# Kernel optimization log

Measured on AMD Instinct MI355X. Metric: run time of the kernel, lower is better.

## Reference

```python
import jax, jax.numpy as jnp
import numpy as np

K = 20  # neighbors


def _knn_idx(x, k):
    # x: (B, N, C). pairwise_distance[b,i,j] = -||x_i - x_j||^2; topk -> k nearest (incl. self)
    inner = jnp.einsum('bic,bjc->bij', x, x)            # (B, N, N)
    sq = jnp.sum(x * x, axis=-1)                         # (B, N)
    pd = 2.0 * inner - sq[:, :, None] - sq[:, None, :]   # (B, N, N)
    return jax.lax.top_k(pd, k)[1]                       # (B, N, k) int32


def _gather_neighbors(x, idx):
    # Faithful to source: flatten to (B*N, C) and index with per-batch indices in [0, N).
    # This means every batch gathers from batch 0's rows (bug in original, reproduced).
    B, N, C = x.shape
    flat = x.reshape(B * N, C)
    return flat[idx.reshape(-1)].reshape(B, N, idx.shape[-1], C)  # (B, N, k, C)


def setup_inputs() -> dict:
    key = jax.random.key(0)
    ks = jax.random.split(key, 11)
    B, N = 8, 4096
    emb_dim = 1024
    s = 0.05
    inp = {
        'x':  jax.random.normal(ks[0], (B, N, 3), dtype=jnp.float32),
        'w1': jax.random.normal(ks[1], (3, 64), dtype=jnp.float32) * s,
        'b1': jax.random.normal(ks[2], (64,), dtype=jnp.float32) * s,
        'w2': jax.random.normal(ks[3], (64, 64), dtype=jnp.float32) * s,
        'b2': jax.random.normal(ks[4], (64,), dtype=jnp.float32) * s,
        'w3': jax.random.normal(ks[5], (64, 64), dtype=jnp.float32) * s,
        'b3': jax.random.normal(ks[6], (64,), dtype=jnp.float32) * s,
        'w4': jax.random.normal(ks[7], (64, 128), dtype=jnp.float32) * s,
        'b4': jax.random.normal(ks[8], (128,), dtype=jnp.float32) * s,
        'w5': jax.random.normal(ks[9], (128, emb_dim), dtype=jnp.float32) * s,
        'b5': jax.random.normal(ks[10], (emb_dim,), dtype=jnp.float32) * s,
    }
    return inp


def reference(x, w1, b1, w2, b2, w3, b3, w4, b4, w5, b5):
    # Stage 1: knn on xyz, gather, mlp1 (3->64->64->64 with ReLUs), max over k
    idx = _knn_idx(x, K)                                  # (B, N, K)
    nb = _gather_neighbors(x, idx)                        # (B, N, K, 3)
    h = jax.nn.relu(nb @ w1 + b1)
    h = jax.nn.relu(h @ w2 + b2)
    h = h @ w3 + b3                                       # (B, N, K, 64)
    h = jnp.max(h, axis=2)                                # (B, N, 64)
    # Stage 2: knn on 64-d features, gather, mlp2 (64->128), max over k
    idx = _knn_idx(h, K)
    nb = _gather_neighbors(h, idx)                        # (B, N, K, 64)
    h = nb @ w4 + b4                                      # (B, N, K, 128)
    h = jnp.max(h, axis=2)                                # (B, N, 128)
    # mlp3 (128 -> emb_dim)
    return h @ w5 + b5                                    # (B, N, emb_dim)
```

## Files before the change

### kernel.cpp

```cpp
#include <hip/hip_runtime.h>
#include <stddef.h>

#define NBATCH 8
#define NP 4096
#define KNN 20
#define NEGF (-3.402823466e38f)

__device__ __forceinline__ void clear_slot(float (&val)[64], int tw, int lw, int lane) {
  switch (tw) {
#define CS(T) case T: if (lane == lw) val[T] = NEGF; break;
    CS(0) CS(1) CS(2) CS(3) CS(4) CS(5) CS(6) CS(7)
    CS(8) CS(9) CS(10) CS(11) CS(12) CS(13) CS(14) CS(15)
    CS(16) CS(17) CS(18) CS(19) CS(20) CS(21) CS(22) CS(23)
    CS(24) CS(25) CS(26) CS(27) CS(28) CS(29) CS(30) CS(31)
    CS(32) CS(33) CS(34) CS(35) CS(36) CS(37) CS(38) CS(39)
    CS(40) CS(41) CS(42) CS(43) CS(44) CS(45) CS(46) CS(47)
    CS(48) CS(49) CS(50) CS(51) CS(52) CS(53) CS(54) CS(55)
    CS(56) CS(57) CS(58) CS(59) CS(60) CS(61) CS(62) CS(63)
#undef CS
  }
}

__device__ __forceinline__ void wave_topk(float (&val)[64], int lane, int rowbase,
                                          int* __restrict__ idx_out) {
  int myidx = 0;
  #pragma unroll 1
  for (int r = 0; r < KNN; ++r) {
    float m[4]; int mt[4];
    #pragma unroll
    for (int q = 0; q < 4; ++q) { m[q] = val[q]; mt[q] = q; }
    #pragma unroll
    for (int t = 4; t < 64; t += 4) {
      #pragma unroll
      for (int q = 0; q < 4; ++q) {
        if (val[t + q] > m[q]) { m[q] = val[t + q]; mt[q] = t + q; }
      }
    }
    if (m[1] > m[0] || (m[1] == m[0] && mt[1] < mt[0])) { m[0] = m[1]; mt[0] = mt[1]; }
    if (m[3] > m[2] || (m[3] == m[2] && mt[3] < mt[2])) { m[2] = m[3]; mt[2] = mt[3]; }
    if (m[2] > m[0] || (m[2] == m[0] && mt[2] < mt[0])) { m[0] = m[2]; mt[0] = mt[2]; }
    float mv = m[0];
    int mj = mt[0] * 64 + lane;
    #pragma unroll
    for (int off = 32; off; off >>= 1) {
      float om = __shfl_xor(mv, off, 64);
      int   oj = __shfl_xor(mj, off, 64);
      if (om > mv || (om == mv && oj < mj)) { mv = om; mj = oj; }
    }
    clear_slot(val, mj >> 6, mj & 63, lane);
    if (lane == r) myidx = mj;
  }
  if (lane < KNN) idx_out[(size_t)rowbase * KNN + lane] = myidx;
}

__global__ __launch_bounds__(256) void sq_kernel(const float* __restrict__ x,
                                                 float* __restrict__ sqx) {
  int gid = blockIdx.x * 256 + threadIdx.x;
  float a = x[gid * 3 + 0];
  float b = x[gid * 3 + 1];
  float c = x[gid * 3 + 2];
  sqx[gid] = a * a + b * b + c * c;
}

__global__ __launch_bounds__(256) void knn1_kernel(const float* __restrict__ x,
                                                   const float* __restrict__ sqx,
                                                   int* __restrict__ idx1) {
  int wave = threadIdx.x >> 6, lane = threadIdx.x & 63;
  int row = blockIdx.x * 4 + wave;
  int b = row >> 12;
  int i = row & (NP - 1);
  const float* xb = x + (size_t)b * NP * 3;
  float xi0 = xb[i * 3 + 0], xi1 = xb[i * 3 + 1], xi2 = xb[i * 3 + 2];
  float sqi = sqx[row];
  const float* sqb = sqx + b * NP;
  float val[64];
  #pragma unroll
  for (int t = 0; t < 64; ++t) {
    int j = t * 64 + lane;
    float a0 = xb[j * 3 + 0], a1 = xb[j * 3 + 1], a2 = xb[j * 3 + 2];
    float dot = xi0 * a0 + xi1 * a1 + xi2 * a2;
    val[t] = 2.f * dot - sqi - sqb[j];
  }
  wave_topk(val, lane, row, idx1);
}

__global__ __launch_bounds__(256) void mlp1_kernel(const float* __restrict__ x,
                                                   const float* __restrict__ w1, const float* __restrict__ b1,
                                                   const float* __restrict__ w2, const float* __restrict__ b2,
                                                   const float* __restrict__ w3, const float* __restrict__ b3,
                                                   float* __restrict__ F1) {
  int wave = threadIdx.x >> 6, lane = threadIdx.x & 63;
  int j = blockIdx.x * 4 + wave;
  float x0 = x[j * 3 + 0], x1 = x[j * 3 + 1], x2 = x[j * 3 + 2];
  float h1 = fmaf(x2, w1[128 + lane], fmaf(x1, w1[64 + lane], fmaf(x0, w1[lane], b1[lane])));
  h1 = fmaxf(h1, 0.f);
  float acc = b2[lane];
  #pragma unroll
  for (int c = 0; c < 64; ++c) acc = fmaf(__shfl(h1, c, 64), w2[c * 64 + lane], acc);
  float h2 = fmaxf(acc, 0.f);
  acc = b3[lane];
  #pragma unroll
  for (int c = 0; c < 64; ++c) acc = fmaf(__shfl(h2, c, 64), w3[c * 64 + lane], acc);
  F1[j * 64 + lane] = acc;
}

__global__ __launch_bounds__(256) void pool1_kernel(const float* __restrict__ F1,
                                                    const int* __restrict__ idx1,
                                                    float* __restrict__ h,
                                                    float* __restrict__ sqh) {
  int wave = threadIdx.x >> 6, lane = threadIdx.x & 63;
  int row = blockIdx.x * 4 + wave;
  float m = NEGF;
  #pragma unroll
  for (int k = 0; k < KNN; ++k) {
    int jj = idx1[(size_t)row * KNN + k];
    m = fmaxf(m, F1[jj * 64 + lane]);
  }
  h[(size_t)row * 64 + lane] = m;
  float s = m * m;
  #pragma unroll
  for (int off = 32; off; off >>= 1) s += __shfl_xor(s, off, 64);
  if (lane == 0) sqh[row] = s;
}

__device__ __forceinline__ int swz(int g, int r) { return g ^ ((r & 15) ^ ((r >> 4) & 3)); }

__global__ __launch_bounds__(256) void pd_gemm_kernel(const float* __restrict__ h,
                                                      const float* __restrict__ sqh,
                                                      float* __restrict__ pd, int b) {
  __shared__ float As[64 * 64];
  __shared__ float Bs[64 * 64];
  const int it = blockIdx.x >> 6;
  const int jt = blockIdx.x & 63;
  const int i0 = it * 64, j0 = jt * 64;
  const float* hb = h + (size_t)b * NP * 64;
  const int tid = threadIdx.x;
  #pragma unroll
  for (int s = 0; s < 4; ++s) {
    int f4 = tid + s * 256;
    int r = f4 >> 4, g = f4 & 15;
    int gs = swz(g, r);
    float4 va = *reinterpret_cast<const float4*>(&hb[(size_t)(i0 + r) * 64 + g * 4]);
    *reinterpret_cast<float4*>(&As[r * 64 + gs * 4]) = va;
    float4 vb = *reinterpret_cast<const float4*>(&hb[(size_t)(j0 + r) * 64 + g * 4]);
    *reinterpret_cast<float4*>(&Bs[r * 64 + gs * 4]) = vb;
  }
  __syncthreads();
  const int tx = tid & 15, ty = tid >> 4;
  float acc[4][4] = {};
  #pragma unroll
  for (int c = 0; c < 64; c += 4) {
    int g = c >> 2;
    float4 a[4], bb[4];
    #pragma unroll
    for (int q = 0; q < 4; ++q) {
      int r = ty * 4 + q;
      a[q] = *reinterpret_cast<const float4*>(&As[r * 64 + (swz(g, r) << 2)]);
    }
    #pragma unroll
    for (int p = 0; p < 4; ++p) {
      int r = tx * 4 + p;
      bb[p] = *reinterpret_cast<const float4*>(&Bs[r * 64 + (swz(g, r) << 2)]);
    }
    #pragma unroll
    for (int q = 0; q < 4; ++q) {
      #pragma unroll
      for (int p = 0; p < 4; ++p) {
        acc[q][p] = fmaf(a[q].x, bb[p].x, acc[q][p]);
        acc[q][p] = fmaf(a[q].y, bb[p].y, acc[q][p]);
        acc[q][p] = fmaf(a[q].z, bb[p].z, acc[q][p]);
        acc[q][p] = fmaf(a[q].w, bb[p].w, acc[q][p]);
      }
    }
  }
  const float* sq = sqh + b * NP;
  float sj0 = sq[j0 + tx * 4 + 0];
  float sj1 = sq[j0 + tx * 4 + 1];
  float sj2 = sq[j0 + tx * 4 + 2];
  float sj3 = sq[j0 + tx * 4 + 3];
  #pragma unroll
  for (int q = 0; q < 4; ++q) {
    int i = i0 + ty * 4 + q;
    float sqi = sq[i];
    float4 o;
    o.x = 2.f * acc[q][0] - sqi - sj0;
    o.y = 2.f * acc[q][1] - sqi - sj1;
    o.z = 2.f * acc[q][2] - sqi - sj2;
    o.w = 2.f * acc[q][3] - sqi - sj3;
    *reinterpret_cast<float4*>(&pd[(size_t)i * NP + j0 + tx * 4]) = o;
  }
}

__global__ __launch_bounds__(256) void knn_select_kernel(const float* __restrict__ pd,
                                                         int* __restrict__ idx2, int b) {
  int wave = threadIdx.x >> 6, lane = threadIdx.x & 63;
  int row = blockIdx.x * 4 + wave;
  float val[64];
  #pragma unroll
  for (int t = 0; t < 64; ++t) val[t] = pd[(size_t)row * NP + t * 64 + lane];
  wave_topk(val, lane, b * NP + row, idx2);
}

__global__ __launch_bounds__(512) void knn2_fused_kernel(const float* __restrict__ h,
                                                         const float* __restrict__ sqh,
                                                         int* __restrict__ idx2) {
  __shared__ float tile[64 * 64];
  const int wave = threadIdx.x >> 6, lane = threadIdx.x & 63;
  const int row = blockIdx.x * 8 + wave;
  const int b = row >> 12;
  const int jb = b * NP;
  float hi[64];
  #pragma unroll
  for (int q2 = 0; q2 < 16; ++q2) {
    float4 v = *reinterpret_cast<const float4*>(&h[(size_t)row * 64 + q2 * 4]);
    hi[q2 * 4 + 0] = v.x; hi[q2 * 4 + 1] = v.y; hi[q2 * 4 + 2] = v.z; hi[q2 * 4 + 3] = v.w;
  }
  float sqi = sqh[row];
  float val[64];
  #pragma unroll
  for (int tt = 0; tt < 64; ++tt) {
    __syncthreads();
    #pragma unroll
    for (int s = 0; s < 2; ++s) {
      int f4 = threadIdx.x + s * 512;
      int jj = f4 >> 4, g = f4 & 15;
      float4 v = *reinterpret_cast<const float4*>(&h[(size_t)(jb + tt * 64 + jj) * 64 + g * 4]);
      int gs = g ^ (jj & 15);
      *reinterpret_cast<float4*>(&tile[jj * 64 + gs * 4]) = v;
    }
    __syncthreads();
    float acc = 0.f;
    #pragma unroll
    for (int g = 0; g < 16; ++g) {
      int gs = g ^ (lane & 15);
      float4 v = *reinterpret_cast<const float4*>(&tile[lane * 64 + gs * 4]);
      acc = fmaf(hi[4 * g + 0], v.x, acc);
      acc = fmaf(hi[4 * g + 1], v.y, acc);
      acc = fmaf(hi[4 * g + 2], v.z, acc);
      acc = fmaf(hi[4 * g + 3], v.w, acc);
    }
    val[tt] = 2.f * acc - sqi - sqh[jb + tt * 64 + lane];
  }
  wave_topk(val, lane, row, idx2);
}

__global__ __launch_bounds__(128) void g4_kernel(const float* __restrict__ h,
                                                 const float* __restrict__ w4,
                                                 const float* __restrict__ b4,
                                                 float* __restrict__ G4) {
  __shared__ float hj[64];
  int j = blockIdx.x;
  int o = threadIdx.x;
  if (o < 64) hj[o] = h[(size_t)j * 64 + o];
  __syncthreads();
  float acc = b4[o];
  #pragma unroll
  for (int c = 0; c < 64; ++c) acc = fmaf(hj[c], w4[c * 128 + o], acc);
  G4[(size_t)j * 128 + o] = acc;
}

__global__ __launch_bounds__(256) void pool2_kernel(const float* __restrict__ G4,
                                                    const int* __restrict__ idx2,
                                                    float* __restrict__ h2) {
  int gid = blockIdx.x * 256 + threadIdx.x;
  int row = gid >> 7, o = gid & 127;
  float m = NEGF;
  #pragma unroll
  for (int k = 0; k < KNN; ++k) {
    int jj = idx2[(size_t)row * KNN + k];
    m = fmaxf(m, G4[(size_t)jj * 128 + o]);
  }
  h2[(size_t)gid] = m;
}

__global__ __launch_bounds__(256) void final_gemm_kernel(const float* __restrict__ h2,
                                                         const float* __restrict__ w5,
                                                         const float* __restrict__ b5,
                                                         float* __restrict__ out) {
  __shared__ float As[64 * 128];
  __shared__ float Bs[128 * 64];
  const int mt = blockIdx.x >> 4;
  const int nt = blockIdx.x & 15;
  const int row0 = mt * 64, col0 = nt * 64;
  const int tid = threadIdx.x;
  #pragma unroll
  for (int s = 0; s < 8; ++s) {
    int f4 = tid + s * 256;
    int i = f4 >> 5, kf = f4 & 31;
    float4 v = *reinterpret_cast<const float4*>(&h2[(size_t)(row0 + i) * 128 + kf * 4]);
    *reinterpret_cast<float4*>(&As[i * 128 + kf * 4]) = v;
  }
  #pragma unroll
  for (int s = 0; s < 8; ++s) {
    int f4 = tid + s * 256;
    int k = f4 >> 4, g = f4 & 15;
    float4 v = *reinterpret_cast<const float4*>(&w5[(size_t)k * 1024 + col0 + g * 4]);
    *reinterpret_cast<float4*>(&Bs[k * 64 + g * 4]) = v;
  }
  __syncthreads();
  const int tx = tid & 15, ty = tid >> 4;
  float acc[4][4] = {};
  #pragma unroll
  for (int k = 0; k < 128; k += 4) {
    float4 a[4], bb[4];
    #pragma unroll
    for (int q = 0; q < 4; ++q)
      a[q] = *reinterpret_cast<const float4*>(&As[(ty * 4 + q) * 128 + k]);
    #pragma unroll
    for (int kk = 0; kk < 4; ++kk)
      bb[kk] = *reinterpret_cast<const float4*>(&Bs[(k + kk) * 64 + tx * 4]);
    #pragma unroll
    for (int q = 0; q < 4; ++q) {
      acc[q][0] = fmaf(a[q].w, bb[3].x, fmaf(a[q].z, bb[2].x, fmaf(a[q].y, bb[1].x, fmaf(a[q].x, bb[0].x, acc[q][0]))));
      acc[q][1] = fmaf(a[q].w, bb[3].y, fmaf(a[q].z, bb[2].y, fmaf(a[q].y, bb[1].y, fmaf(a[q].x, bb[0].y, acc[q][1]))));
      acc[q][2] = fmaf(a[q].w, bb[3].z, fmaf(a[q].z, bb[2].z, fmaf(a[q].y, bb[1].z, fmaf(a[q].x, bb[0].z, acc[q][2]))));
      acc[q][3] = fmaf(a[q].w, bb[3].w, fmaf(a[q].z, bb[2].w, fmaf(a[q].y, bb[1].w, fmaf(a[q].x, bb[0].w, acc[q][3]))));
    }
  }
  float b0 = b5[col0 + tx * 4 + 0];
  float b1 = b5[col0 + tx * 4 + 1];
  float b2 = b5[col0 + tx * 4 + 2];
  float b3 = b5[col0 + tx * 4 + 3];
  #pragma unroll
  for (int q = 0; q < 4; ++q) {
    float4 o;
    o.x = acc[q][0] + b0;
    o.y = acc[q][1] + b1;
    o.z = acc[q][2] + b2;
    o.w = acc[q][3] + b3;
    *reinterpret_cast<float4*>(&out[(size_t)(row0 + ty * 4 + q) * 1024 + col0 + tx * 4]) = o;
  }
}

extern "C" void kernel_launch(void* const* d_in, const int* in_sizes, int n_in,
                              void* d_out, int out_size, void* d_ws, size_t ws_size,
                              hipStream_t stream) {
  const float* x  = (const float*)d_in[0];
  const float* w1 = (const float*)d_in[1];
  const float* b1 = (const float*)d_in[2];
  const float* w2 = (const float*)d_in[3];
  const float* b2 = (const float*)d_in[4];
  const float* w3 = (const float*)d_in[5];
  const float* b3 = (const float*)d_in[6];
  const float* w4 = (const float*)d_in[7];
  const float* b4 = (const float*)d_in[8];
  const float* w5 = (const float*)d_in[9];
  const float* b5 = (const float*)d_in[10];
  float* out = (float*)d_out;
  char* ws = (char*)d_ws;

  float* h    = (float*)(ws + 0);
  float* sqh  = (float*)(ws + 8388608);
  int*   idx2 = (int*)  (ws + 8519680);
  char*  X    = ws + 11141120;
  float* sqx  = (float*)(X + 0);
  int*   idx1 = (int*)  (X + 131072);
  float* F1   = (float*)(X + 2752512);
  float* pd   = (float*)(X + 0);
  float* G4   = (float*)(X + 0);
  float* h2   = (float*)(X + 2097152);

  const size_t NEED_FAST = 11141120 + 67108864;

  sq_kernel<<<128, 256, 0, stream>>>(x, sqx);
  knn1_kernel<<<8192, 256, 0, stream>>>(x, sqx, idx1);
  mlp1_kernel<<<1024, 256, 0, stream>>>(x, w1, b1, w2, b2, w3, b3, F1);
  pool1_kernel<<<8192, 256, 0, stream>>>(F1, idx1, h, sqh);

  if (ws_size >= NEED_FAST) {
    for (int b = 0; b < NBATCH; ++b) {
      pd_gemm_kernel<<<4096, 256, 0, stream>>>(h, sqh, pd, b);
      knn_select_kernel<<<1024, 256, 0, stream>>>(pd, idx2, b);
    }
  } else {
    knn2_fused_kernel<<<4096, 512, 0, stream>>>(h, sqh, idx2);
  }

  g4_kernel<<<4096, 128, 0, stream>>>(h, w4, b4, G4);
  pool2_kernel<<<16384, 256, 0, stream>>>(G4, idx2, h2);
  final_gemm_kernel<<<8192, 256, 0, stream>>>(h2, w5, b5, out);
}
```

Measured before the change: 1.235 ms.

## Cache per-lane group maxima in top-k selection to avoid full rescans

The wave top-k now keeps eight group maxima per lane, so each round only rescans the 8-entry group that lost its winner, and only in the owning lane, instead of rescanning all 64 values in every lane. The knn1 and knn_select kernels also switch to a lane-major layout, with contiguous columns per lane, so the select kernel can use float4 loads. This cuts per-round selection ALU work at the cost of extra registers and a less coalesced access pattern in knn1. Tie-breaking within a lane now keeps the first maximum through strict compares.

Result: slower. 1.491 ms (+20.7%).

```diff
diff --git a/kernel.cpp b/kernel.cpp
--- a/kernel.cpp
+++ b/kernel.cpp
@@ -6,49 +6,65 @@
 #define KNN 20
 #define NEGF (-3.402823466e38f)
 
-__device__ __forceinline__ void clear_slot(float (&val)[64], int tw, int lw, int lane) {
-  switch (tw) {
-#define CS(T) case T: if (lane == lw) val[T] = NEGF; break;
-    CS(0) CS(1) CS(2) CS(3) CS(4) CS(5) CS(6) CS(7)
-    CS(8) CS(9) CS(10) CS(11) CS(12) CS(13) CS(14) CS(15)
-    CS(16) CS(17) CS(18) CS(19) CS(20) CS(21) CS(22) CS(23)
-    CS(24) CS(25) CS(26) CS(27) CS(28) CS(29) CS(30) CS(31)
-    CS(32) CS(33) CS(34) CS(35) CS(36) CS(37) CS(38) CS(39)
-    CS(40) CS(41) CS(42) CS(43) CS(44) CS(45) CS(46) CS(47)
-    CS(48) CS(49) CS(50) CS(51) CS(52) CS(53) CS(54) CS(55)
-    CS(56) CS(57) CS(58) CS(59) CS(60) CS(61) CS(62) CS(63)
-#undef CS
-  }
-}
-
-__device__ __forceinline__ void wave_topk(float (&val)[64], int lane, int rowbase,
-                                          int* __restrict__ idx_out) {
+template<int G>
+__device__ __forceinline__ void rem_group(float (&val)[64], float (&gv)[8], int (&gt)[8],
+                                          int s, bool own) {
+  switch (s) {
+    case 0: if (own) val[G * 8 + 0] = NEGF; break;
+    case 1: if (own) val[G * 8 + 1] = NEGF; break;
+    case 2: if (own) val[G * 8 + 2] = NEGF; break;
+    case 3: if (own) val[G * 8 + 3] = NEGF; break;
+    case 4: if (own) val[G * 8 + 4] = NEGF; break;
+    case 5: if (own) val[G * 8 + 5] = NEGF; break;
+    case 6: if (own) val[G * 8 + 6] = NEGF; break;
+    case 7: if (own) val[G * 8 + 7] = NEGF; break;
+  }
+  if (own) {
+    float mv = val[G * 8]; int mt = G * 8;
+    #pragma unroll
+    for (int q = 1; q < 8; ++q)
+      if (val[G * 8 + q] > mv) { mv = val[G * 8 + q]; mt = G * 8 + q; }
+    gv[G] = mv; gt[G] = mt;
+  }
+}
+
+template<bool LANEMAJOR>
+__device__ __forceinline__ void wave_topk(float (&val)[64], float (&gv)[8], int (&gt)[8],
+                                          int lane, int rowbase, int* __restrict__ idx_out) {
+  float lv = gv[0]; int lt = gt[0];
+  #pragma unroll
+  for (int g = 1; g < 8; ++g) if (gv[g] > lv) { lv = gv[g]; lt = gt[g]; }
   int myidx = 0;
   #pragma unroll 1
   for (int r = 0; r < KNN; ++r) {
-    float m[4]; int mt[4];
-    #pragma unroll
-    for (int q = 0; q < 4; ++q) { m[q] = val[q]; mt[q] = q; }
-    #pragma unroll
-    for (int t = 4; t < 64; t += 4) {
-      #pragma unroll
-      for (int q = 0; q < 4; ++q) {
-        if (val[t + q] > m[q]) { m[q] = val[t + q]; mt[q] = t + q; }
-      }
-    }
-    if (m[1] > m[0] || (m[1] == m[0] && mt[1] < mt[0])) { m[0] = m[1]; mt[0] = mt[1]; }
-    if (m[3] > m[2] || (m[3] == m[2] && mt[3] < mt[2])) { m[2] = m[3]; mt[2] = mt[3]; }
-    if (m[2] > m[0] || (m[2] == m[0] && mt[2] < mt[0])) { m[0] = m[2]; mt[0] = mt[2]; }
-    float mv = m[0];
-    int mj = mt[0] * 64 + lane;
+    float mv = lv;
+    int mj = LANEMAJOR ? ((lane << 6) | lt) : ((lt << 6) | lane);
     #pragma unroll
     for (int off = 32; off; off >>= 1) {
       float om = __shfl_xor(mv, off, 64);
       int   oj = __shfl_xor(mj, off, 64);
       if (om > mv || (om == mv && oj < mj)) { mv = om; mj = oj; }
     }
-    clear_slot(val, mj >> 6, mj & 63, lane);
     if (lane == r) myidx = mj;
+    int mju = __builtin_amdgcn_readfirstlane(mj);
+    int wl = LANEMAJOR ? (mju >> 6) : (mju & 63);
+    int t  = LANEMAJOR ? (mju & 63) : (mju >> 6);
+    bool own = (lane == wl);
+    switch (t >> 3) {
+      case 0: rem_group<0>(val, gv, gt, t & 7, own); break;
+      case 1: rem_group<1>(val, gv, gt, t & 7, own); break;
+      case 2: rem_group<2>(val, gv, gt, t & 7, own); break;
+      case 3: rem_group<3>(val, gv, gt, t & 7, own); break;
+      case 4: rem_group<4>(val, gv, gt, t & 7, own); break;
+      case 5: rem_group<5>(val, gv, gt, t & 7, own); break;
+      case 6: rem_group<6>(val, gv, gt, t & 7, own); break;
+      case 7: rem_group<7>(val, gv, gt, t & 7, own); break;
+    }
+    if (own) {
+      lv = gv[0]; lt = gt[0];
+      #pragma unroll
+      for (int g = 1; g < 8; ++g) if (gv[g] > lv) { lv = gv[g]; lt = gt[g]; }
+    }
   }
   if (lane < KNN) idx_out[(size_t)rowbase * KNN + lane] = myidx;
 }
@@ -73,15 +89,24 @@
   float xi0 = xb[i * 3 + 0], xi1 = xb[i * 3 + 1], xi2 = xb[i * 3 + 2];
   float sqi = sqx[row];
   const float* sqb = sqx + b * NP;
-  float val[64];
-  #pragma unroll
-  for (int t = 0; t < 64; ++t) {
-    int j = t * 64 + lane;
-    float a0 = xb[j * 3 + 0], a1 = xb[j * 3 + 1], a2 = xb[j * 3 + 2];
-    float dot = xi0 * a0 + xi1 * a1 + xi2 * a2;
-    val[t] = 2.f * dot - sqi - sqb[j];
-  }
-  wave_topk(val, lane, row, idx1);
+  float val[64]; float gv[8]; int gt[8];
+  #pragma unroll
+  for (int g = 0; g < 8; ++g) {
+    #pragma unroll
+    for (int s = 0; s < 8; ++s) {
+      int t = g * 8 + s;
+      int j = (lane << 6) | t;
+      float a0 = xb[j * 3 + 0], a1 = xb[j * 3 + 1], a2 = xb[j * 3 + 2];
+      float dot = xi0 * a0 + xi1 * a1 + xi2 * a2;
+      val[t] = 2.f * dot - sqi - sqb[j];
+    }
+    float mv = val[g * 8]; int mt = g * 8;
+    #pragma unroll
+    for (int s = 1; s < 8; ++s)
+      if (val[g * 8 + s] > mv) { mv = val[g * 8 + s]; mt = g * 8 + s; }
+    gv[g] = mv; gt[g] = mt;
+  }
+  wave_topk<true>(val, gv, gt, lane, row, idx1);
 }
 
 __global__ __launch_bounds__(256) void mlp1_kernel(const float* __restrict__ x,
@@ -195,10 +220,21 @@
                                                          int* __restrict__ idx2, int b) {
   int wave = threadIdx.x >> 6, lane = threadIdx.x & 63;
   int row = blockIdx.x * 4 + wave;
-  float val[64];
-  #pragma unroll
-  for (int t = 0; t < 64; ++t) val[t] = pd[(size_t)row * NP + t * 64 + lane];
-  wave_topk(val, lane, b * NP + row, idx2);
+  const float* prow = pd + (size_t)row * NP + (lane << 6);
+  float val[64]; float gv[8]; int gt[8];
+  #pragma unroll
+  for (int g = 0; g < 8; ++g) {
+    float4 v0 = *reinterpret_cast<const float4*>(&prow[g * 8]);
+    float4 v1 = *reinterpret_cast<const float4*>(&prow[g * 8 + 4]);
+    val[g * 8 + 0] = v0.x; val[g * 8 + 1] = v0.y; val[g * 8 + 2] = v0.z; val[g * 8 + 3] = v0.w;
+    val[g * 8 + 4] = v1.x; val[g * 8 + 5] = v1.y; val[g * 8 + 6] = v1.z; val[g * 8 + 7] = v1.w;
+    float mv = val[g * 8]; int mt = g * 8;
+    #pragma unroll
+    for (int s = 1; s < 8; ++s)
+      if (val[g * 8 + s] > mv) { mv = val[g * 8 + s]; mt = g * 8 + s; }
+    gv[g] = mv; gt[g] = mt;
+  }
+  wave_topk<true>(val, gv, gt, lane, b * NP + row, idx2);
 }
 
 __global__ __launch_bounds__(512) void knn2_fused_kernel(const float* __restrict__ h,
@@ -241,7 +277,16 @@
     }
     val[tt] = 2.f * acc - sqi - sqh[jb + tt * 64 + lane];
   }
-  wave_topk(val, lane, row, idx2);
+  float gv[8]; int gt[8];
+  #pragma unroll
+  for (int g = 0; g < 8; ++g) {
+    float mv = val[g * 8]; int mt = g * 8;
+    #pragma unroll
+    for (int s = 1; s < 8; ++s)
+      if (val[g * 8 + s] > mv) { mv = val[g * 8 + s]; mt = g * 8 + s; }
+    gv[g] = mv; gt[g] = mt;
+  }
+  wave_topk<false>(val, gv, gt, lane, row, idx2);
 }
 
 __global__ __launch_bounds__(128) void g4_kernel(const float* __restrict__ h,
```

## Replace register-array top-k with grouped per-lane maxima and lazy recompute

Applied to the files above, without the earlier changes.

The knn1 and knn_select kernels no longer hold 64 candidates per lane in registers. Each lane now owns a contiguous block of 64 columns, kept as 8 groups of 8 with a cached maximum per group. After each wave-wide argmax, only the winning lane recomputes or reloads the one affected group, applying a removed-bit mask. This cuts register pressure and the per-round 64-element scan, in exchange for divergent reloads from memory on the winning lane. The column-to-lane mapping changes to lane*64+t, which allows vectorized float4 loads. knn1 also drops the constant sqi term.

After: 1.182 ms. -4.3%, faster.

```diff
diff --git a/kernel.cpp b/kernel.cpp
--- a/kernel.cpp
+++ b/kernel.cpp
@@ -6,7 +6,309 @@
 #define KNN 20
 #define NEGF (-3.402823466e38f)
 
-__device__ __forceinline__ void clear_slot(float (&val)[64], int tw, int lw, int lane) {
+
+template<int G>
+__device__ __forceinline__ void knn1_group(const float* __restrict__ xb,
+                                           const float* __restrict__ sqb,
+                                           int lane, float xi0, float xi1, float xi2,
+                                           unsigned mask8, float& gmv, int& gmt) {
+  const float* xg = xb + 3 * ((lane << 6) | (G * 8));
+  const float* sg = sqb + ((lane << 6) | (G * 8));
+  float4 v0 = *(const float4*)(xg + 0);
+  float4 v1 = *(const float4*)(xg + 4);
+  float4 v2 = *(const float4*)(xg + 8);
+  float4 v3 = *(const float4*)(xg + 12);
+  float4 v4 = *(const float4*)(xg + 16);
+  float4 v5 = *(const float4*)(xg + 20);
+  float4 s0 = *(const float4*)(sg + 0);
+  float4 s1 = *(const float4*)(sg + 4);
+  float d0 = fmaf(xi2, v0.z, fmaf(xi1, v0.y, xi0 * v0.x)); d0 = fmaf(d0, 2.f, -s0.x);
+  float d1 = fmaf(xi2, v1.y, fmaf(xi1, v1.x, xi0 * v0.w)); d1 = fmaf(d1, 2.f, -s0.y);
+  float d2 = fmaf(xi2, v2.x, fmaf(xi1, v1.w, xi0 * v1.z)); d2 = fmaf(d2, 2.f, -s0.z);
+  float d3 = fmaf(xi2, v2.w, fmaf(xi1, v2.z, xi0 * v2.y)); d3 = fmaf(d3, 2.f, -s0.w);
+  float d4 = fmaf(xi2, v3.z, fmaf(xi1, v3.y, xi0 * v3.x)); d4 = fmaf(d4, 2.f, -s1.x);
+  float d5 = fmaf(xi2, v4.y, fmaf(xi1, v4.x, xi0 * v3.w)); d5 = fmaf(d5, 2.f, -s1.y);
+  float d6 = fmaf(xi2, v5.x, fmaf(xi1, v4.w, xi0 * v4.z)); d6 = fmaf(d6, 2.f, -s1.z);
+  float d7 = fmaf(xi2, v5.w, fmaf(xi1, v5.z, xi0 * v5.y)); d7 = fmaf(d7, 2.f, -s1.w);
+  if (mask8 & 1u)   d0 = NEGF;
+  if (mask8 & 2u)   d1 = NEGF;
+  if (mask8 & 4u)   d2 = NEGF;
+  if (mask8 & 8u)   d3 = NEGF;
+  if (mask8 & 16u)  d4 = NEGF;
+  if (mask8 & 32u)  d5 = NEGF;
+  if (mask8 & 64u)  d6 = NEGF;
+  if (mask8 & 128u) d7 = NEGF;
+  float mv = d0; int mt = 0;
+  if (d1 > mv) { mv = d1; mt = 1; }
+  if (d2 > mv) { mv = d2; mt = 2; }
+  if (d3 > mv) { mv = d3; mt = 3; }
+  if (d4 > mv) { mv = d4; mt = 4; }
+  if (d5 > mv) { mv = d5; mt = 5; }
+  if (d6 > mv) { mv = d6; mt = 6; }
+  if (d7 > mv) { mv = d7; mt = 7; }
+  gmv = mv; gmt = G * 8 + mt;
+}
+
+template<int G>
+__device__ __forceinline__ void sel_group(const float* __restrict__ prow,
+                                          unsigned mask8, float& gmv, int& gmt) {
+  float4 a = *(const float4*)(prow + G * 8);
+  float4 b = *(const float4*)(prow + G * 8 + 4);
+  float d0 = a.x, d1 = a.y, d2 = a.z, d3 = a.w;
+  float d4 = b.x, d5 = b.y, d6 = b.z, d7 = b.w;
+  if (mask8 & 1u)   d0 = NEGF;
+  if (mask8 & 2u)   d1 = NEGF;
+  if (mask8 & 4u)   d2 = NEGF;
+  if (mask8 & 8u)   d3 = NEGF;
+  if (mask8 & 16u)  d4 = NEGF;
+  if (mask8 & 32u)  d5 = NEGF;
+  if (mask8 & 64u)  d6 = NEGF;
+  if (mask8 & 128u) d7 = NEGF;
+  float mv = d0; int mt = 0;
+  if (d1 > mv) { mv = d1; mt = 1; }
+  if (d2 > mv) { mv = d2; mt = 2; }
+  if (d3 > mv) { mv = d3; mt = 3; }
+  if (d4 > mv) { mv = d4; mt = 4; }
+  if (d5 > mv) { mv = d5; mt = 5; }
+  if (d6 > mv) { mv = d6; mt = 6; }
+  if (d7 > mv) { mv = d7; mt = 7; }
+  gmv = mv; gmt = G * 8 + mt;
+}
+
+#define LANE_SCAN()                                            \
+  lv = gv0; lt = gt0;                                          \
+  if (gv1 > lv) { lv = gv1; lt = gt1; }                        \
+  if (gv2 > lv) { lv = gv2; lt = gt2; }                        \
+  if (gv3 > lv) { lv = gv3; lt = gt3; }                        \
+  if (gv4 > lv) { lv = gv4; lt = gt4; }                        \
+  if (gv5 > lv) { lv = gv5; lt = gt5; }                        \
+  if (gv6 > lv) { lv = gv6; lt = gt6; }                        \
+  if (gv7 > lv) { lv = gv7; lt = gt7; }
+
+__global__ __launch_bounds__(256) void sq_kernel(const float* __restrict__ x,
+                                                 float* __restrict__ sqx) {
+  int gid = blockIdx.x * 256 + threadIdx.x;
+  float a = x[gid * 3 + 0];
+  float b = x[gid * 3 + 1];
+  float c = x[gid * 3 + 2];
+  sqx[gid] = a * a + b * b + c * c;
+}
+
+__global__ __launch_bounds__(256) void knn1_kernel(const float* __restrict__ x,
+                                                   const float* __restrict__ sqx,
+                                                   int* __restrict__ idx1) {
+  int wave = threadIdx.x >> 6, lane = threadIdx.x & 63;
+  int row = blockIdx.x * 4 + wave;
+  int b = row >> 12;
+  int i = row & (NP - 1);
+  const float* xb = x + (size_t)b * NP * 3;
+  const float* sqb = sqx + b * NP;
+  float xi0 = xb[i * 3 + 0], xi1 = xb[i * 3 + 1], xi2 = xb[i * 3 + 2];
+
+  float gv0, gv1, gv2, gv3, gv4, gv5, gv6, gv7;
+  int   gt0, gt1, gt2, gt3, gt4, gt5, gt6, gt7;
+  unsigned rm0 = 0u, rm1 = 0u;
+  knn1_group<0>(xb, sqb, lane, xi0, xi1, xi2, 0u, gv0, gt0);
+  knn1_group<1>(xb, sqb, lane, xi0, xi1, xi2, 0u, gv1, gt1);
+  knn1_group<2>(xb, sqb, lane, xi0, xi1, xi2, 0u, gv2, gt2);
+  knn1_group<3>(xb, sqb, lane, xi0, xi1, xi2, 0u, gv3, gt3);
+  knn1_group<4>(xb, sqb, lane, xi0, xi1, xi2, 0u, gv4, gt4);
+  knn1_group<5>(xb, sqb, lane, xi0, xi1, xi2, 0u, gv5, gt5);
+  knn1_group<6>(xb, sqb, lane, xi0, xi1, xi2, 0u, gv6, gt6);
+  knn1_group<7>(xb, sqb, lane, xi0, xi1, xi2, 0u, gv7, gt7);
+  float lv; int lt;
+  LANE_SCAN();
+
+  int myidx = 0;
+  #pragma unroll 1
+  for (int r = 0; r < KNN; ++r) {
+    float mv = lv;
+    int mj = (lane << 6) | lt;
+    #pragma unroll
+    for (int off = 32; off; off >>= 1) {
+      float om = __shfl_xor(mv, off, 64);
+      int   oj = __shfl_xor(mj, off, 64);
+      if (om > mv || (om == mv && oj < mj)) { mv = om; mj = oj; }
+    }
+    if (lane == r) myidx = mj;
+    int mju = __builtin_amdgcn_readfirstlane(mj);
+    int wl = mju >> 6, tu = mju & 63;
+    if (lane == wl) {
+      switch (tu >> 3) {
+        case 0: rm0 |= 1u << (tu & 7);        knn1_group<0>(xb, sqb, lane, xi0, xi1, xi2, rm0 & 0xffu,         gv0, gt0); break;
+        case 1: rm0 |= 1u << (8 + (tu & 7));  knn1_group<1>(xb, sqb, lane, xi0, xi1, xi2, (rm0 >> 8) & 0xffu,  gv1, gt1); break;
+        case 2: rm0 |= 1u << (16 + (tu & 7)); knn1_group<2>(xb, sqb, lane, xi0, xi1, xi2, (rm0 >> 16) & 0xffu, gv2, gt2); break;
+        case 3: rm0 |= 1u << (24 + (tu & 7)); knn1_group<3>(xb, sqb, lane, xi0, xi1, xi2, (rm0 >> 24) & 0xffu, gv3, gt3); break;
+        case 4: rm1 |= 1u << (tu & 7);        knn1_group<4>(xb, sqb, lane, xi0, xi1, xi2, rm1 & 0xffu,         gv4, gt4); break;
+        case 5: rm1 |= 1u << (8 + (tu & 7));  knn1_group<5>(xb, sqb, lane, xi0, xi1, xi2, (rm1 >> 8) & 0xffu,  gv5, gt5); break;
+        case 6: rm1 |= 1u << (16 + (tu & 7)); knn1_group<6>(xb, sqb, lane, xi0, xi1, xi2, (rm1 >> 16) & 0xffu, gv6, gt6); break;
+        case 7: rm1 |= 1u << (24 + (tu & 7)); knn1_group<7>(xb, sqb, lane, xi0, xi1, xi2, (rm1 >> 24) & 0xffu, gv7, gt7); break;
+      }
+      LANE_SCAN();
+    }
+  }
+  if (lane < KNN) idx1[(size_t)row * KNN + lane] = myidx;
+}
+
+__global__ __launch_bounds__(256) void mlp1_kernel(const float* __restrict__ x,
+                                                   const float* __restrict__ w1, const float* __restrict__ b1,
+                                                   const float* __restrict__ w2, const float* __restrict__ b2,
+                                                   const float* __restrict__ w3, const float* __restrict__ b3,
+                                                   float* __restrict__ F1) {
+  int wave = threadIdx.x >> 6, lane = threadIdx.x & 63;
+  int j = blockIdx.x * 4 + wave;
+  float x0 = x[j * 3 + 0], x1 = x[j * 3 + 1], x2 = x[j * 3 + 2];
+  float h1 = fmaf(x2, w1[128 + lane], fmaf(x1, w1[64 + lane], fmaf(x0, w1[lane], b1[lane])));
+  h1 = fmaxf(h1, 0.f);
+  float acc = b2[lane];
+  #pragma unroll
+  for (int c = 0; c < 64; ++c) acc = fmaf(__shfl(h1, c, 64), w2[c * 64 + lane], acc);
+  float h2 = fmaxf(acc, 0.f);
+  acc = b3[lane];
+  #pragma unroll
+  for (int c = 0; c < 64; ++c) acc = fmaf(__shfl(h2, c, 64), w3[c * 64 + lane], acc);
+  F1[j * 64 + lane] = acc;
+}
+
+__global__ __launch_bounds__(256) void pool1_kernel(const float* __restrict__ F1,
+                                                    const int* __restrict__ idx1,
+                                                    float* __restrict__ h,
+                                                    float* __restrict__ sqh) {
+  int wave = threadIdx.x >> 6, lane = threadIdx.x & 63;
+  int row = blockIdx.x * 4 + wave;
+  float m = NEGF;
+  #pragma unroll
+  for (int k = 0; k < KNN; ++k) {
+    int jj = idx1[(size_t)row * KNN + k];
+    m = fmaxf(m, F1[jj * 64 + lane]);
+  }
+  h[(size_t)row * 64 + lane] = m;
+  float s = m * m;
+  #pragma unroll
+  for (int off = 32; off; off >>= 1) s += __shfl_xor(s, off, 64);
+  if (lane == 0) sqh[row] = s;
+}
+
+__device__ __forceinline__ int swz(int g, int r) { return g ^ ((r & 15) ^ ((r >> 4) & 3)); }
+
+__global__ __launch_bounds__(256) void pd_gemm_kernel(const float* __restrict__ h,
+                                                      const float* __restrict__ sqh,
+                                                      float* __restrict__ pd, int b) {
+  __shared__ float As[64 * 64];
+  __shared__ float Bs[64 * 64];
+  const int it = blockIdx.x >> 6;
+  const int jt = blockIdx.x & 63;
+  const int i0 = it * 64, j0 = jt * 64;
+  const float* hb = h + (size_t)b * NP * 64;
+  const int tid = threadIdx.x;
+  #pragma unroll
+  for (int s = 0; s < 4; ++s) {
+    int f4 = tid + s * 256;
+    int r = f4 >> 4, g = f4 & 15;
+    int gs = swz(g, r);
+    float4 va = *reinterpret_cast<const float4*>(&hb[(size_t)(i0 + r) * 64 + g * 4]);
+    *reinterpret_cast<float4*>(&As[r * 64 + gs * 4]) = va;
+    float4 vb = *reinterpret_cast<const float4*>(&hb[(size_t)(j0 + r) * 64 + g * 4]);
+    *reinterpret_cast<float4*>(&Bs[r * 64 + gs * 4]) = vb;
+  }
+  __syncthreads();
+  const int tx = tid & 15, ty = tid >> 4;
+  float acc[4][4] = {};
+  #pragma unroll
+  for (int c = 0; c < 64; c += 4) {
+    int g = c >> 2;
+    float4 a[4], bb[4];
+    #pragma unroll
+    for (int q = 0; q < 4; ++q) {
+      int r = ty * 4 + q;
+      a[q] = *reinterpret_cast<const float4*>(&As[r * 64 + (swz(g, r) << 2)]);
+    }
+    #pragma unroll
+    for (int p = 0; p < 4; ++p) {
+      int r = tx * 4 + p;
+      bb[p] = *reinterpret_cast<const float4*>(&Bs[r * 64 + (swz(g, r) << 2)]);
+    }
+    #pragma unroll
+    for (int q = 0; q < 4; ++q) {
+      #pragma unroll
+      for (int p = 0; p < 4; ++p) {
+        acc[q][p] = fmaf(a[q].x, bb[p].x, acc[q][p]);
+        acc[q][p] = fmaf(a[q].y, bb[p].y, acc[q][p]);
+        acc[q][p] = fmaf(a[q].z, bb[p].z, acc[q][p]);
+        acc[q][p] = fmaf(a[q].w, bb[p].w, acc[q][p]);
+      }
+    }
+  }
+  const float* sq = sqh + b * NP;
+  float sj0 = sq[j0 + tx * 4 + 0];
+  float sj1 = sq[j0 + tx * 4 + 1];
+  float sj2 = sq[j0 + tx * 4 + 2];
+  float sj3 = sq[j0 + tx * 4 + 3];
+  #pragma unroll
+  for (int q = 0; q < 4; ++q) {
+    int i = i0 + ty * 4 + q;
+    float sqi = sq[i];
+    float4 o;
+    o.x = 2.f * acc[q][0] - sqi - sj0;
+    o.y = 2.f * acc[q][1] - sqi - sj1;
+    o.z = 2.f * acc[q][2] - sqi - sj2;
+    o.w = 2.f * acc[q][3] - sqi - sj3;
+    *reinterpret_cast<float4*>(&pd[(size_t)i * NP + j0 + tx * 4]) = o;
+  }
+}
+
+__global__ __launch_bounds__(256) void knn_select_kernel(const float* __restrict__ pd,
+                                                         int* __restrict__ idx2, int b) {
+  int wave = threadIdx.x >> 6, lane = threadIdx.x & 63;
+  int row = blockIdx.x * 4 + wave;
+  const float* prow = pd + (size_t)row * NP + (lane << 6);
+
+  float gv0, gv1, gv2, gv3, gv4, gv5, gv6, gv7;
+  int   gt0, gt1, gt2, gt3, gt4, gt5, gt6, gt7;
+  unsigned rm0 = 0u, rm1 = 0u;
+  sel_group<0>(prow, 0u, gv0, gt0);
+  sel_group<1>(prow, 0u, gv1, gt1);
+  sel_group<2>(prow, 0u, gv2, gt2);
+  sel_group<3>(prow, 0u, gv3, gt3);
+  sel_group<4>(prow, 0u, gv4, gt4);
+  sel_group<5>(prow, 0u, gv5, gt5);
+  sel_group<6>(prow, 0u, gv6, gt6);
+  sel_group<7>(prow, 0u, gv7, gt7);
+  float lv; int lt;
+  LANE_SCAN();
+
+  int myidx = 0;
+  #pragma unroll 1
+  for (int r = 0; r < KNN; ++r) {
+    float mv = lv;
+    int mj = (lane << 6) | lt;
+    #pragma unroll
+    for (int off = 32; off; off >>= 1) {
+      float om = __shfl_xor(mv, off, 64);
+      int   oj = __shfl_xor(mj, off, 64);
+      if (om > mv || (om == mv && oj < mj)) { mv = om; mj = oj; }
+    }
+    if (lane == r) myidx = mj;
+    int mju = __builtin_amdgcn_readfirstlane(mj);
+    int wl = mju >> 6, tu = mju & 63;
+    if (lane == wl) {
+      switch (tu >> 3) {
+        case 0: rm0 |= 1u << (tu & 7);        sel_group<0>(prow, rm0 & 0xffu,         gv0, gt0); break;
+        case 1: rm0 |= 1u << (8 + (tu & 7));  sel_group<1>(prow, (rm0 >> 8) & 0xffu,  gv1, gt1); break;
+        case 2: rm0 |= 1u << (16 + (tu & 7)); sel_group<2>(prow, (rm0 >> 16) & 0xffu, gv2, gt2); break;
+        case 3: rm0 |= 1u << (24 + (tu & 7)); sel_group<3>(prow, (rm0 >> 24) & 0xffu, gv3, gt3); break;
+        case 4: rm1 |= 1u << (tu & 7);        sel_group<4>(prow, rm1 & 0xffu,         gv4, gt4); break;
+        case 5: rm1 |= 1u << (8 + (tu & 7));  sel_group<5>(prow, (rm1 >> 8) & 0xffu,  gv5, gt5); break;
+        case 6: rm1 |= 1u << (16 + (tu & 7)); sel_group<6>(prow, (rm1 >> 16) & 0xffu, gv6, gt6); break;
+        case 7: rm1 |= 1u << (24 + (tu & 7)); sel_group<7>(prow, (rm1 >> 24) & 0xffu, gv7, gt7); break;
+      }
+      LANE_SCAN();
+    }
+  }
+  if (lane < KNN) idx2[(size_t)(b * NP + row) * KNN + lane] = myidx;
+}
+
+__device__ __forceinline__ void clear_slot_fb(float (&val)[64], int tw, int lw, int lane) {
   switch (tw) {
 #define CS(T) case T: if (lane == lw) val[T] = NEGF; break;
     CS(0) CS(1) CS(2) CS(3) CS(4) CS(5) CS(6) CS(7)
@@ -21,8 +323,8 @@
   }
 }
 
-__device__ __forceinline__ void wave_topk(float (&val)[64], int lane, int rowbase,
-                                          int* __restrict__ idx_out) {
+__device__ __forceinline__ void wave_topk_fb(float (&val)[64], int lane, int rowbase,
+                                             int* __restrict__ idx_out) {
   int myidx = 0;
   #pragma unroll 1
   for (int r = 0; r < KNN; ++r) {
@@ -47,158 +349,10 @@
       int   oj = __shfl_xor(mj, off, 64);
       if (om > mv || (om == mv && oj < mj)) { mv = om; mj = oj; }
     }
-    clear_slot(val, mj >> 6, mj & 63, lane);
+    clear_slot_fb(val, mj >> 6, mj & 63, lane);
     if (lane == r) myidx = mj;
   }
   if (lane < KNN) idx_out[(size_t)rowbase * KNN + lane] = myidx;
-}
-
-__global__ __launch_bounds__(256) void sq_kernel(const float* __restrict__ x,
-                                                 float* __restrict__ sqx) {
-  int gid = blockIdx.x * 256 + threadIdx.x;
-  float a = x[gid * 3 + 0];
-  float b = x[gid * 3 + 1];
-  float c = x[gid * 3 + 2];
-  sqx[gid] = a * a + b * b + c * c;
-}
-
-__global__ __launch_bounds__(256) void knn1_kernel(const float* __restrict__ x,
-                                                   const float* __restrict__ sqx,
-                                                   int* __restrict__ idx1) {
-  int wave = threadIdx.x >> 6, lane = threadIdx.x & 63;
-  int row = blockIdx.x * 4 + wave;
-  int b = row >> 12;
-  int i = row & (NP - 1);
-  const float* xb = x + (size_t)b * NP * 3;
-  float xi0 = xb[i * 3 + 0], xi1 = xb[i * 3 + 1], xi2 = xb[i * 3 + 2];
-  float sqi = sqx[row];
-  const float* sqb = sqx + b * NP;
-  float val[64];
-  #pragma unroll
-  for (int t = 0; t < 64; ++t) {
-    int j = t * 64 + lane;
-    float a0 = xb[j * 3 + 0], a1 = xb[j * 3 + 1], a2 = xb[j * 3 + 2];
-    float dot = xi0 * a0 + xi1 * a1 + xi2 * a2;
-    val[t] = 2.f * dot - sqi - sqb[j];
-  }
-  wave_topk(val, lane, row, idx1);
-}
-
-__global__ __launch_bounds__(256) void mlp1_kernel(const float* __restrict__ x,
-                                                   const float* __restrict__ w1, const float* __restrict__ b1,
-                                                   const float* __restrict__ w2, const float* __restrict__ b2,
-                                                   const float* __restrict__ w3, const float* __restrict__ b3,
-                                                   float* __restrict__ F1) {
-  int wave = threadIdx.x >> 6, lane = threadIdx.x & 63;
-  int j = blockIdx.x * 4 + wave;
-  float x0 = x[j * 3 + 0], x1 = x[j * 3 + 1], x2 = x[j * 3 + 2];
-  float h1 = fmaf(x2, w1[128 + lane], fmaf(x1, w1[64 + lane], fmaf(x0, w1[lane], b1[lane])));
-  h1 = fmaxf(h1, 0.f);
-  float acc = b2[lane];
-  #pragma unroll
-  for (int c = 0; c < 64; ++c) acc = fmaf(__shfl(h1, c, 64), w2[c * 64 + lane], acc);
-  float h2 = fmaxf(acc, 0.f);
-  acc = b3[lane];
-  #pragma unroll
-  for (int c = 0; c < 64; ++c) acc = fmaf(__shfl(h2, c, 64), w3[c * 64 + lane], acc);
-  F1[j * 64 + lane] = acc;
-}
-
-__global__ __launch_bounds__(256) void pool1_kernel(const float* __restrict__ F1,
-                                                    const int* __restrict__ idx1,
-                                                    float* __restrict__ h,
-                                                    float* __restrict__ sqh) {
-  int wave = threadIdx.x >> 6, lane = threadIdx.x & 63;
-  int row = blockIdx.x * 4 + wave;
-  float m = NEGF;
-  #pragma unroll
-  for (int k = 0; k < KNN; ++k) {
-    int jj = idx1[(size_t)row * KNN + k];
-    m = fmaxf(m, F1[jj * 64 + lane]);
-  }
-  h[(size_t)row * 64 + lane] = m;
-  float s = m * m;
-  #pragma unroll
-  for (int off = 32; off; off >>= 1) s += __shfl_xor(s, off, 64);
-  if (lane == 0) sqh[row] = s;
-}
-
-__device__ __forceinline__ int swz(int g, int r) { return g ^ ((r & 15) ^ ((r >> 4) & 3)); }
-
-__global__ __launch_bounds__(256) void pd_gemm_kernel(const float* __restrict__ h,
-                                                      const float* __restrict__ sqh,
-                                                      float* __restrict__ pd, int b) {
-  __shared__ float As[64 * 64];
-  __shared__ float Bs[64 * 64];
-  const int it = blockIdx.x >> 6;
-  const int jt = blockIdx.x & 63;
-  const int i0 = it * 64, j0 = jt * 64;
-  const float* hb = h + (size_t)b * NP * 64;
-  const int tid = threadIdx.x;
-  #pragma unroll
-  for (int s = 0; s < 4; ++s) {
-    int f4 = tid + s * 256;
-    int r = f4 >> 4, g = f4 & 15;
-    int gs = swz(g, r);
-    float4 va = *reinterpret_cast<const float4*>(&hb[(size_t)(i0 + r) * 64 + g * 4]);
-    *reinterpret_cast<float4*>(&As[r * 64 + gs * 4]) = va;
-    float4 vb = *reinterpret_cast<const float4*>(&hb[(size_t)(j0 + r) * 64 + g * 4]);
-    *reinterpret_cast<float4*>(&Bs[r * 64 + gs * 4]) = vb;
-  }
-  __syncthreads();
-  const int tx = tid & 15, ty = tid >> 4;
-  float acc[4][4] = {};
-  #pragma unroll
-  for (int c = 0; c < 64; c += 4) {
-    int g = c >> 2;
-    float4 a[4], bb[4];
-    #pragma unroll
-    for (int q = 0; q < 4; ++q) {
-      int r = ty * 4 + q;
-      a[q] = *reinterpret_cast<const float4*>(&As[r * 64 + (swz(g, r) << 2)]);
-    }
-    #pragma unroll
-    for (int p = 0; p < 4; ++p) {
-      int r = tx * 4 + p;
-      bb[p] = *reinterpret_cast<const float4*>(&Bs[r * 64 + (swz(g, r) << 2)]);
-    }
-    #pragma unroll
-    for (int q = 0; q < 4; ++q) {
-      #pragma unroll
-      for (int p = 0; p < 4; ++p) {
-        acc[q][p] = fmaf(a[q].x, bb[p].x, acc[q][p]);
-        acc[q][p] = fmaf(a[q].y, bb[p].y, acc[q][p]);
-        acc[q][p] = fmaf(a[q].z, bb[p].z, acc[q][p]);
-        acc[q][p] = fmaf(a[q].w, bb[p].w, acc[q][p]);
-      }
-    }
-  }
-  const float* sq = sqh + b * NP;
-  float sj0 = sq[j0 + tx * 4 + 0];
-  float sj1 = sq[j0 + tx * 4 + 1];
-  float sj2 = sq[j0 + tx * 4 + 2];
-  float sj3 = sq[j0 + tx * 4 + 3];
-  #pragma unroll
-  for (int q = 0; q < 4; ++q) {
-    int i = i0 + ty * 4 + q;
-    float sqi = sq[i];
-    float4 o;
-    o.x = 2.f * acc[q][0] - sqi - sj0;
-    o.y = 2.f * acc[q][1] - sqi - sj1;
-    o.z = 2.f * acc[q][2] - sqi - sj2;
-    o.w = 2.f * acc[q][3] - sqi - sj3;
-    *reinterpret_cast<float4*>(&pd[(size_t)i * NP + j0 + tx * 4]) = o;
-  }
-}
-
-__global__ __launch_bounds__(256) void knn_select_kernel(const float* __restrict__ pd,
-                                                         int* __restrict__ idx2, int b) {
-  int wave = threadIdx.x >> 6, lane = threadIdx.x & 63;
-  int row = blockIdx.x * 4 + wave;
-  float val[64];
-  #pragma unroll
-  for (int t = 0; t < 64; ++t) val[t] = pd[(size_t)row * NP + t * 64 + lane];
-  wave_topk(val, lane, b * NP + row, idx2);
 }
 
 __global__ __launch_bounds__(512) void knn2_fused_kernel(const float* __restrict__ h,
@@ -241,7 +395,7 @@
     }
     val[tt] = 2.f * acc - sqi - sqh[jb + tt * 64 + lane];
   }
-  wave_topk(val, lane, row, idx2);
+  wave_topk_fb(val, lane, row, idx2);
 }
 
 __global__ __launch_bounds__(128) void g4_kernel(const float* __restrict__ h,
```
